# Kernel tuning notes

Measured on AMD Instinct MI355X. Metric: run time of the kernel, lower is better.

The kernel has to match this reference:

```python
import jax, jax.numpy as jnp
import numpy as np

N_QUBITS = 8
N_LAYERS = 3
N_FEATURES = 16
BATCH = 65536
DIM = 2 ** N_QUBITS  # 256 amplitudes
EPS = 1e-5  # torch BatchNorm1d default eps

# Precompute CNOT permutations (wire 0 = most significant bit, PennyLane order)
_idx = np.arange(DIM)
CNOT_PERMS = []
for _i in range(N_QUBITS):
    for _j in range(_i + 1, N_QUBITS):
        _c = (_idx >> (N_QUBITS - 1 - _i)) & 1
        CNOT_PERMS.append(np.where(_c == 1, _idx ^ (1 << (N_QUBITS - 1 - _j)), _idx))
# PauliZ sign table: (DIM, N_QUBITS), +1 for bit 0, -1 for bit 1
Z_SIGNS = np.stack([1.0 - 2.0 * ((_idx >> (N_QUBITS - 1 - i)) & 1) for i in range(N_QUBITS)], axis=1).astype(np.float32)


def _ry(theta):
    t = jnp.asarray(theta)
    c = jnp.cos(t / 2).astype(jnp.complex64)
    s = jnp.sin(t / 2).astype(jnp.complex64)
    return jnp.stack([jnp.stack([c, -s], -1), jnp.stack([s, c], -1)], -2)


def _rx(theta):
    t = jnp.asarray(theta)
    c = jnp.cos(t / 2).astype(jnp.complex64)
    s = (-1j) * jnp.sin(t / 2).astype(jnp.complex64)
    return jnp.stack([jnp.stack([c, s], -1), jnp.stack([s, c], -1)], -2)


def _rz(theta):
    e = jnp.exp(-0.5j * jnp.asarray(theta, jnp.complex64))
    z = jnp.zeros_like(e)
    return jnp.stack([jnp.stack([e, z], -1), jnp.stack([z, jnp.conj(e)], -1)], -2)


def _apply_1q(state, U, w):
    # state: (B, DIM); U: (2,2) shared or (B,2,2) per-sample; wire w
    B = state.shape[0]
    left, right = 2 ** w, 2 ** (N_QUBITS - 1 - w)
    s = state.reshape(B, left, 2, right)
    if U.ndim == 2:
        out = jnp.einsum('st,bpsq->bptq', U, s)
    else:
        out = jnp.einsum('bst,bpsq->bptq', U, s)
    return out.reshape(B, DIM)


def _quantum(angles, qw):
    # Batched state-vector simulation of the PennyLane circuit.
    # angles: (B, N_QUBITS) float32 encoding angles; qw: (N_LAYERS, N_QUBITS, 3)
    B = angles.shape[0]
    state = jnp.zeros((B, DIM), jnp.complex64).at[:, 0].set(1.0 + 0.0j)
    for i in range(N_QUBITS):  # RY(inputs[i]) encoding, per-sample angles
        state = _apply_1q(state, _ry(angles[:, i]), i)
    for l in range(N_LAYERS):
        for i in range(N_QUBITS):
            state = _apply_1q(state, _rx(qw[l, i, 0]), i)
            state = _apply_1q(state, _ry(qw[l, i, 1]), i)
            state = _apply_1q(state, _rz(qw[l, i, 2]), i)
        for perm in CNOT_PERMS:  # all-pairs CNOT(i, j), i < j
            state = state[:, perm]
    probs = state.real ** 2 + state.imag ** 2  # (B, DIM)
    return probs @ jnp.asarray(Z_SIGNS)  # (B, N_QUBITS) <Z_i> expectations


def _bn(h, g, b, m, v):
    # BatchNorm1d in inference mode (running stats)
    return (h - m) * jax.lax.rsqrt(v + EPS) * g + b


def _forward(x, W1, b1, g1, bt1, m1, v1, W2, b2, g2, bt2, m2, v2, W3, b3, q_weights, W4, b4, g4, bt4, m4, v4, W5, b5, W6, b6):
    h = jax.nn.relu(_bn(x @ W1.T + b1, g1, bt1, m1, v1))
    h = jax.nn.relu(_bn(h @ W2.T + b2, g2, bt2, m2, v2))
    pre = jnp.tanh(h @ W3.T + b3)  # (B, N_QUBITS)
    # Original detaches before the quantum circuit -> no grad through it
    q_out = _quantum(jax.lax.stop_gradient(pre), jax.lax.stop_gradient(q_weights))
    h = jax.nn.relu(_bn(q_out @ W4.T + b4, g4, bt4, m4, v4))
    h = jax.nn.relu(h @ W5.T + b5)
    return h @ W6.T + b6  # (B, 1)


def setup_inputs() -> dict:
    key = jax.random.key(0)
    ks = jax.random.split(key, 8)

    def lin(k, o, i):
        return (jax.random.normal(k, (o, i), jnp.float32) / np.sqrt(i)).astype(jnp.float32)

    return {
        'x': jax.random.normal(ks[0], (BATCH, N_FEATURES), jnp.float32),
        'W1': lin(ks[1], 128, N_FEATURES), 'b1': jnp.zeros((128,), jnp.float32),
        'g1': jnp.ones((128,), jnp.float32), 'bt1': jnp.zeros((128,), jnp.float32),
        'm1': jnp.zeros((128,), jnp.float32), 'v1': jnp.ones((128,), jnp.float32),
        'W2': lin(ks[2], 64, 128), 'b2': jnp.zeros((64,), jnp.float32),
        'g2': jnp.ones((64,), jnp.float32), 'bt2': jnp.zeros((64,), jnp.float32),
        'm2': jnp.zeros((64,), jnp.float32), 'v2': jnp.ones((64,), jnp.float32),
        'W3': lin(ks[3], N_QUBITS, 64), 'b3': jnp.zeros((N_QUBITS,), jnp.float32),
        'q_weights': jax.random.normal(ks[4], (N_LAYERS, N_QUBITS, 3), jnp.float32) * 0.1,
        'W4': lin(ks[5], 32, N_QUBITS), 'b4': jnp.zeros((32,), jnp.float32),
        'g4': jnp.ones((32,), jnp.float32), 'bt4': jnp.zeros((32,), jnp.float32),
        'm4': jnp.zeros((32,), jnp.float32), 'v4': jnp.ones((32,), jnp.float32),
        'W5': lin(ks[6], 16, 32), 'b5': jnp.zeros((16,), jnp.float32),
        'W6': lin(ks[7], 1, 16), 'b6': jnp.zeros((1,), jnp.float32),
    }


def reference(x, W1, b1, g1, bt1, m1, v1, W2, b2, g2, bt2, m2, v2, W3, b3, q_weights, W4, b4, g4, bt4, m4, v4, W5, b5, W6, b6):
    return _forward(x, W1, b1, g1, bt1, m1, v1, W2, b2, g2, bt2, m2, v2, W3, b3, q_weights, W4, b4, g4, bt4, m4, v4, W5, b5, W6, b6)
```

## Files before the change

kernel.cpp:

```cpp
#include <hip/hip_runtime.h>

__device__ __forceinline__ float2 cmul(float2 a, float2 b){
    return make_float2(a.x*b.x - a.y*b.y, a.x*b.y + a.y*b.x);
}
__device__ __forceinline__ float2 cadd(float2 a, float2 b){
    return make_float2(a.x + b.x, a.y + b.y);
}
__device__ __forceinline__ unsigned short f2h(float f){
    _Float16 h = (_Float16)f;
    return __builtin_bit_cast(unsigned short, h);
}

typedef _Float16 f16x8 __attribute__((ext_vector_type(8)));
typedef float    f32x4 __attribute__((ext_vector_type(4)));

__device__ __forceinline__ void split8(const float* p, f16x8& ah, f16x8& al){
    const f32x4* q = (const f32x4*)p;
    f32x4 v0 = q[0], v1 = q[1];
    float av[8] = {v0[0],v0[1],v0[2],v0[3],v1[0],v1[1],v1[2],v1[3]};
    #pragma unroll
    for (int j=0;j<8;++j){
        _Float16 h = (_Float16)av[j];
        ah[j] = h;
        al[j] = (_Float16)(av[j] - (float)h);
    }
}

__device__ __forceinline__ void build_gates(const float* qw, int l, int c, float2 (*G)[2][2]){
    if (c < 8){
        int i = c;
        float t0 = 0.5f*qw[l*24 + i*3 + 0];
        float t1 = 0.5f*qw[l*24 + i*3 + 1];
        float t2 = 0.5f*qw[l*24 + i*3 + 2];
        float c1,s1,c2,s2,c3,s3;
        sincosf(t0,&s1,&c1); sincosf(t1,&s2,&c2); sincosf(t2,&s3,&c3);
        float2 RX[2][2] = {{{c1,0.f},{0.f,-s1}},{{0.f,-s1},{c1,0.f}}};
        float2 RY[2][2] = {{{c2,0.f},{s2,0.f}},{{-s2,0.f},{c2,0.f}}};
        float2 M[2][2];
        #pragma unroll
        for (int r=0;r<2;++r)
            #pragma unroll
            for (int cc=0;cc<2;++cc)
                M[r][cc] = cadd(cmul(RY[r][0],RX[0][cc]), cmul(RY[r][1],RX[1][cc]));
        float2 e  = {c3,-s3};
        float2 ec = {c3, s3};
        G[i][0][0]=cmul(e, M[0][0]); G[i][0][1]=cmul(e, M[0][1]);
        G[i][1][0]=cmul(ec,M[1][0]); G[i][1][1]=cmul(ec,M[1][1]);
    }
}
__device__ __forceinline__ int cnot_perm(int k){
    int r = k;
    for (int i=6;i>=0;--i)
        for (int j=7;j>i;--j)
            if ((r >> (7-i)) & 1) r ^= 1 << (7-j);
    return r;
}

__global__ void k_build_prep(const float* __restrict__ qw, float2* __restrict__ U,
                       const float* __restrict__ W1, const float* __restrict__ b1,
                       const float* __restrict__ g1, const float* __restrict__ bt1,
                       const float* __restrict__ m1, const float* __restrict__ v1,
                       const float* __restrict__ W2, const float* __restrict__ b2,
                       const float* __restrict__ g2, const float* __restrict__ bt2,
                       const float* __restrict__ m2, const float* __restrict__ v2,
                       const float* __restrict__ W3,
                       unsigned short* __restrict__ H1w, float* __restrict__ c1,
                       unsigned short* __restrict__ H2w, float* __restrict__ c2,
                       unsigned short* __restrict__ H3w){
    if (blockIdx.y == 2){
        if (blockIdx.x >= 8) return;
        int tid = blockIdx.x*256 + threadIdx.x;
        const int stride = 8*256;
        for (int i=tid; i<4096; i+=stride){ int n=i>>5, k=i&31;
            float s=g1[n]*rsqrtf(v1[n]+1e-5f);
            H1w[i] = f2h(k<16 ? W1[n*16+k]*s : 0.f); }
        for (int i=tid; i<128;  i+=stride){ float s=g1[i]*rsqrtf(v1[i]+1e-5f); c1[i]=(b1[i]-m1[i])*s+bt1[i]; }
        for (int i=tid; i<8192; i+=stride){ int n=i>>7;
            float s=g2[n]*rsqrtf(v2[n]+1e-5f);
            H2w[i] = f2h(W2[i]*s); }
        for (int i=tid; i<64;   i+=stride){ float s=g2[i]*rsqrtf(v2[i]+1e-5f); c2[i]=(b2[i]-m2[i])*s+bt2[i]; }
        for (int i=tid; i<1024; i+=stride){ int n=i>>6, k=i&63;
            H3w[i] = f2h(n<8 ? W3[n*64+k] : 0.f); }
        return;
    }
    __shared__ float2 G[8][2][2];
    int l = blockIdx.y, k = blockIdx.x, c = threadIdx.x;
    build_gates(qw, l, c, G);
    __syncthreads();
    int r = cnot_perm(k);
    float2 p = {1.f, 0.f};
    #pragma unroll
    for (int i=0;i<8;++i)
        p = cmul(p, G[i][(r>>(7-i))&1][(c>>(7-i))&1]);
    U[l*65536 + k*256 + c] = p;
}

__global__ __launch_bounds__(256) void k_rowmm(const float* __restrict__ qw,
                                              const float2* __restrict__ U,
                                              unsigned short* __restrict__ WqS){
    __shared__ float2 G[8][2][2];
    __shared__ float2 vs[256];
    __shared__ float2 ws[256];
    int r = blockIdx.x, c = threadIdx.x;
    build_gates(qw, 2, c, G);
    __syncthreads();
    int pr = cnot_perm(r);
    float2 p = {1.f, 0.f};
    #pragma unroll
    for (int i=0;i<8;++i)
        p = cmul(p, G[i][(pr>>(7-i))&1][(c>>(7-i))&1]);
    vs[c] = p;
    __syncthreads();
    float2 acc = {0.f,0.f};
    #pragma unroll 8
    for (int m=0;m<256;++m)
        acc = cadd(acc, cmul(vs[m], U[65536 + m*256 + c]));
    ws[c] = acc;
    __syncthreads();
    float2 z = {0.f,0.f};
    #pragma unroll 8
    for (int m=0;m<256;++m)
        z = cadd(z, cmul(ws[m], U[m*256 + c]));
    int T = r >> 4, l15 = r & 15;
    int ks = c >> 5, lq = (c >> 3) & 3, j = c & 7;
    int lane = lq*16 + l15;
    WqS[((T     *8 + ks)*64 + lane)*8 + j] = f2h(z.x);
    WqS[(((T+16)*8 + ks)*64 + lane)*8 + j] = f2h(z.y);
}

__global__ __launch_bounds__(256,2) void k_front(
    const float* __restrict__ x,
    const unsigned short* __restrict__ H1w, const float* __restrict__ c1,
    const unsigned short* __restrict__ H2w, const float* __restrict__ c2,
    const unsigned short* __restrict__ H3w, const float* __restrict__ b3,
    float* __restrict__ pre)
{
    __shared__ __align__(16) char smem[60416];
    float* XS = (float*)smem;
    float* H1 = (float*)(smem + 9216);
    float* H2 = (float*)(smem + 43008);

    int tid = threadIdx.x;
    int row0 = blockIdx.x*64;
    {
        int r = tid >> 2, q = tid & 3;
        const float4* xp = (const float4*)(x + (row0 + r)*16 + q*4);
        float4 v = xp[0];
        *(float4*)(XS + r*36 + q*4) = v;
        *(float4*)(XS + r*36 + 16 + q*4) = make_float4(0.f,0.f,0.f,0.f);
    }
    __syncthreads();

    int wave = tid>>6, lane = tid&63, l15 = lane&15, lq = lane>>4;
    const f32x4 zz = {0.f,0.f,0.f,0.f};

    f32x4 acc1[4][2];
    #pragma unroll
    for (int mt=0;mt<4;++mt){ acc1[mt][0]=zz; acc1[mt][1]=zz; }
    #pragma unroll
    for (int mt=0; mt<4; ++mt){
        f16x8 ah, al;
        split8(XS + (mt*16+l15)*36 + lq*8, ah, al);
        #pragma unroll
        for (int t=0;t<2;++t){
            int nt = wave + t*4;
            f16x8 b = *(const f16x8*)(H1w + (nt*16+l15)*32 + lq*8);
            acc1[mt][t] = __builtin_amdgcn_mfma_f32_16x16x32_f16(ah, b, acc1[mt][t], 0,0,0);
            acc1[mt][t] = __builtin_amdgcn_mfma_f32_16x16x32_f16(al, b, acc1[mt][t], 0,0,0);
        }
    }
    #pragma unroll
    for (int t=0;t<2;++t){
        int n = (wave + t*4)*16 + l15;
        float bias = c1[n];
        #pragma unroll
        for (int mt=0; mt<4; ++mt)
            #pragma unroll
            for (int reg=0; reg<4; ++reg){
                int rowl = mt*16 + lq*4 + reg;
                H1[rowl*132 + n] = fmaxf(acc1[mt][t][reg] + bias, 0.f);
            }
    }
    __syncthreads();

    f32x4 acc2[4];
    #pragma unroll
    for (int mt=0;mt<4;++mt) acc2[mt]=zz;
    #pragma unroll
    for (int ks=0; ks<4; ++ks){
        f16x8 b = *(const f16x8*)(H2w + (wave*16+l15)*128 + ks*32 + lq*8);
        #pragma unroll
        for (int mt=0; mt<4; ++mt){
            f16x8 ah, al;
            split8(H1 + (mt*16+l15)*132 + ks*32 + lq*8, ah, al);
            acc2[mt] = __builtin_amdgcn_mfma_f32_16x16x32_f16(ah, b, acc2[mt], 0,0,0);
            acc2[mt] = __builtin_amdgcn_mfma_f32_16x16x32_f16(al, b, acc2[mt], 0,0,0);
        }
    }
    {
        int n = wave*16 + l15;
        float bias = c2[n];
        #pragma unroll
        for (int mt=0; mt<4; ++mt)
            #pragma unroll
            for (int reg=0; reg<4; ++reg){
                int rowl = mt*16 + lq*4 + reg;
                H2[rowl*68 + n] = fmaxf(acc2[mt][reg] + bias, 0.f);
            }
    }
    __syncthreads();

    f32x4 acc3 = zz;
    #pragma unroll
    for (int ks=0; ks<2; ++ks){
        f16x8 b = *(const f16x8*)(H3w + l15*64 + ks*32 + lq*8);
        f16x8 ah, al;
        split8(H2 + (wave*16+l15)*68 + ks*32 + lq*8, ah, al);
        acc3 = __builtin_amdgcn_mfma_f32_16x16x32_f16(ah, b, acc3, 0,0,0);
        acc3 = __builtin_amdgcn_mfma_f32_16x16x32_f16(al, b, acc3, 0,0,0);
    }
    if (l15 < 8){
        float bias = b3[l15];
        #pragma unroll
        for (int reg=0; reg<4; ++reg){
            int rowl = wave*16 + lq*4 + reg;
            pre[(row0+rowl)*8 + l15] = tanhf(acc3[reg] + bias);
        }
    }
}

#define A_STRIDE 264
#define P_STRIDE 268
__global__ __launch_bounds__(256,2) void k_main(
    const float* __restrict__ pre, const unsigned short* __restrict__ WqS,
    const float* __restrict__ W4, const float* __restrict__ b4, const float* __restrict__ g4,
    const float* __restrict__ bt4, const float* __restrict__ m4, const float* __restrict__ v4,
    const float* __restrict__ W5, const float* __restrict__ b5,
    const float* __restrict__ W6, const float* __restrict__ b6,
    float* __restrict__ out)
{
    __shared__ __align__(16) char smem[34304 + 4096 + 2048];
    unsigned short* As = (unsigned short*)smem;
    float* probs = (float*)smem;
    float* qacc  = (float*)(smem + 34304);
    float* qout  = (float*)(smem + 34304 + 4096);

    int tid = threadIdx.x;
    {
        int row = tid & 63, q = tid >> 6;
        int grow = blockIdx.x*64 + row;
        const float4* p4 = (const float4*)(pre + grow*8);
        float4 pa = p4[0], pb = p4[1];
        float th[8] = {pa.x,pa.y,pa.z,pa.w,pb.x,pb.y,pb.z,pb.w};
        float cs[8], sn[8];
        #pragma unroll
        for (int i=0;i<8;++i){ __sincosf(0.5f*th[i], &sn[i], &cs[i]); sn[i] = -sn[i]; }
        float F = (q&2 ? sn[0] : cs[0]) * (q&1 ? sn[1] : cs[1]);
        float Pm[8], Pl[8];
        #pragma unroll
        for (int a2=0;a2<8;++a2){
            Pm[a2] = (a2&4?sn[2]:cs[2]) * (a2&2?sn[3]:cs[3]) * (a2&1?sn[4]:cs[4]);
            Pl[a2] = (a2&4?sn[5]:cs[5]) * (a2&2?sn[6]:cs[6]) * (a2&1?sn[7]:cs[7]);
        }
        unsigned short* arow = As + row*A_STRIDE + q*64;
        #pragma unroll
        for (int mh=0;mh<8;++mh){
            float fm = F * Pm[mh];
            uint4 w;
            w.x = (unsigned)f2h(fm*Pl[0]) | ((unsigned)f2h(fm*Pl[1])<<16);
            w.y = (unsigned)f2h(fm*Pl[2]) | ((unsigned)f2h(fm*Pl[3])<<16);
            w.z = (unsigned)f2h(fm*Pl[4]) | ((unsigned)f2h(fm*Pl[5])<<16);
            w.w = (unsigned)f2h(fm*Pl[6]) | ((unsigned)f2h(fm*Pl[7])<<16);
            *reinterpret_cast<uint4*>(arow + mh*8) = w;
        }
    }
    __syncthreads();

    int wave = tid >> 6, lane = tid & 63;
    int l15 = lane & 15, lq = lane >> 4;

    const f16x8* Bp[8];
    #pragma unroll
    for (int t=0;t<8;++t){
        int T = ((t>>2)<<4) + wave*4 + (t&3);
        Bp[t] = reinterpret_cast<const f16x8*>(WqS + T*4096) + lane;
    }
    const f16x8* Ap[4];
    #pragma unroll
    for (int mt=0;mt<4;++mt)
        Ap[mt] = reinterpret_cast<const f16x8*>(As + (mt*16 + l15)*A_STRIDE + lq*8);

    f32x4 acc[4][8];
    const f32x4 zz = {0.f,0.f,0.f,0.f};
    #pragma unroll
    for (int mt=0;mt<4;++mt)
        #pragma unroll
        for (int t=0;t<8;++t) acc[mt][t] = zz;

    f16x8 bfr[2][8];
    #pragma unroll
    for (int t=0;t<8;++t) bfr[0][t] = Bp[t][0];

    #pragma unroll
    for (int ks=0;ks<8;++ks){
        int cur = ks & 1;
        if (ks < 7){
            #pragma unroll
            for (int t=0;t<8;++t) bfr[cur^1][t] = Bp[t][(ks+1)*64];
        }
        f16x8 afr[4];
        #pragma unroll
        for (int mt=0;mt<4;++mt) afr[mt] = Ap[mt][ks*4];
        #pragma unroll
        for (int mt=0;mt<4;++mt)
            #pragma unroll
            for (int t=0;t<8;++t)
                acc[mt][t] = __builtin_amdgcn_mfma_f32_16x16x32_f16(afr[mt], bfr[cur][t], acc[mt][t], 0, 0, 0);
    }
    __syncthreads();

    #pragma unroll
    for (int h=0; h<2; ++h){
        #pragma unroll
        for (int mtl=0; mtl<2; ++mtl){
            int mt = h*2 + mtl;
            #pragma unroll
            for (int t=0;t<4;++t){
                #pragma unroll
                for (int reg=0;reg<4;++reg){
                    float sr = acc[mt][t][reg];
                    float si = acc[mt][t+4][reg];
                    int prow = mtl*16 + lq*4 + reg;
                    int pcol = wave*64 + t*16 + l15;
                    probs[prow*P_STRIDE + pcol] = fmaf(sr,sr,si*si);
                }
            }
        }
        __syncthreads();
        if (tid < 128){
            int row = tid & 31, kg = tid >> 5;
            const float* pb = probs + row*P_STRIDE + kg*64;
            float S=0.f,q2=0.f,q3=0.f,q4=0.f,q5=0.f,q6=0.f,q7=0.f;
            #pragma unroll
            for (int j=0;j<64;++j){
                float p = pb[j];
                S  += p;
                q2 += (j&32)? -p : p;
                q3 += (j&16)? -p : p;
                q4 += (j&8) ? -p : p;
                q5 += (j&4) ? -p : p;
                q6 += (j&2) ? -p : p;
                q7 += (j&1) ? -p : p;
            }
            float* qa = qacc + tid*8;
            qa[0] = (kg&2)? -S : S;
            qa[1] = (kg&1)? -S : S;
            qa[2]=q2; qa[3]=q3; qa[4]=q4; qa[5]=q5; qa[6]=q6; qa[7]=q7;
        }
        __syncthreads();
        {
            int r = tid >> 3, i = tid & 7;
            float v = qacc[r*8+i] + qacc[(32+r)*8+i] + qacc[(64+r)*8+i] + qacc[(96+r)*8+i];
            qout[(h*32 + r)*8 + i] = v;
        }
    }
    __syncthreads();

    if (tid < 64){
        int r = tid;
        float qv[8];
        #pragma unroll
        for (int i=0;i<8;++i) qv[i] = qout[r*8+i];
        float h4[32];
        #pragma unroll
        for (int j=0;j<32;++j){
            float a = b4[j];
            #pragma unroll
            for (int i=0;i<8;++i) a = fmaf(qv[i], W4[j*8+i], a);
            float sc = g4[j]*rsqrtf(v4[j]+1e-5f);
            a = fmaf(a - m4[j], sc, bt4[j]);
            h4[j] = fmaxf(a, 0.f);
        }
        float h5[16];
        #pragma unroll
        for (int j=0;j<16;++j){
            float a = b5[j];
            #pragma unroll
            for (int k=0;k<32;++k) a = fmaf(h4[k], W5[j*32+k], a);
            h5[j] = fmaxf(a, 0.f);
        }
        float o = b6[0];
        #pragma unroll
        for (int k=0;k<16;++k) o = fmaf(h5[k], W6[k], o);
        out[blockIdx.x*64 + r] = o;
    }
}

extern "C" void kernel_launch(void* const* d_in, const int* in_sizes, int n_in,
                              void* d_out, int out_size, void* d_ws, size_t ws_size,
                              hipStream_t stream) {
    (void)in_sizes; (void)n_in; (void)out_size; (void)ws_size;
    const float* x   = (const float*)d_in[0];
    const float* W1  = (const float*)d_in[1];
    const float* b1  = (const float*)d_in[2];
    const float* g1  = (const float*)d_in[3];
    const float* bt1 = (const float*)d_in[4];
    const float* m1  = (const float*)d_in[5];
    const float* v1  = (const float*)d_in[6];
    const float* W2  = (const float*)d_in[7];
    const float* b2  = (const float*)d_in[8];
    const float* g2  = (const float*)d_in[9];
    const float* bt2 = (const float*)d_in[10];
    const float* m2  = (const float*)d_in[11];
    const float* v2  = (const float*)d_in[12];
    const float* W3  = (const float*)d_in[13];
    const float* b3  = (const float*)d_in[14];
    const float* qw  = (const float*)d_in[15];
    const float* W4  = (const float*)d_in[16];
    const float* b4  = (const float*)d_in[17];
    const float* g4  = (const float*)d_in[18];
    const float* bt4 = (const float*)d_in[19];
    const float* m4  = (const float*)d_in[20];
    const float* v4  = (const float*)d_in[21];
    const float* W5  = (const float*)d_in[22];
    const float* b5  = (const float*)d_in[23];
    const float* W6  = (const float*)d_in[24];
    const float* b6  = (const float*)d_in[25];

    char* ws = (char*)d_ws;
    float2* U   = (float2*)ws;
    unsigned short* WqS = (unsigned short*)(U + 2*65536);
    float* pre  = (float*)(WqS + 512*256);
    unsigned short* H1w = (unsigned short*)(pre + 65536*8);
    unsigned short* H2w = H1w + 4096;
    unsigned short* H3w = H2w + 8192;
    float* c1 = (float*)(H3w + 1024);
    float* c2 = c1 + 128;

    k_build_prep<<<dim3(256,3), 256, 0, stream>>>(qw, U,
                                  W1,b1,g1,bt1,m1,v1, W2,b2,g2,bt2,m2,v2, W3,
                                  H1w,c1,H2w,c2,H3w);
    k_rowmm<<<256, 256, 0, stream>>>(qw, U, WqS);
    k_front<<<1024, 256, 0, stream>>>(x, H1w,c1, H2w,c2, H3w,b3, pre);
    k_main<<<1024, 256, 0, stream>>>(pre, WqS, W4,b4,g4,bt4,m4,v4, W5,b5,W6,b6,
                                     (float*)d_out);
}
```

Before: 183.3 us.

## Fuse front MLP and quantum main kernels into one kernel

Merges k_front and k_main into a single kernel that keeps the tanh encoding angles in shared memory, so the intermediate pre buffer no longer makes a round trip through global memory and one launch is dropped. Shared memory is aliased across stages, which needs extra barriers. The PauliZ reduction now uses all 256 threads over 32-column chunks with vector stores and an 8-way sum. The risks are higher LDS use (about 62KB per block), which may limit occupancy, and a longer kernel with more register pressure.

```diff
diff --git a/kernel.cpp b/kernel.cpp
--- a/kernel.cpp
+++ b/kernel.cpp
@@ -128,20 +128,35 @@
     WqS[(((T+16)*8 + ks)*64 + lane)*8 + j] = f2h(z.y);
 }
 
-__global__ __launch_bounds__(256,2) void k_front(
+#define A_STRIDE 264
+#define P_STRIDE 269
+__global__ __launch_bounds__(256,2) void k_fused(
     const float* __restrict__ x,
     const unsigned short* __restrict__ H1w, const float* __restrict__ c1,
     const unsigned short* __restrict__ H2w, const float* __restrict__ c2,
     const unsigned short* __restrict__ H3w, const float* __restrict__ b3,
-    float* __restrict__ pre)
+    const unsigned short* __restrict__ WqS,
+    const float* __restrict__ W4, const float* __restrict__ b4, const float* __restrict__ g4,
+    const float* __restrict__ bt4, const float* __restrict__ m4, const float* __restrict__ v4,
+    const float* __restrict__ W5, const float* __restrict__ b5,
+    const float* __restrict__ W6, const float* __restrict__ b6,
+    float* __restrict__ out)
 {
-    __shared__ __align__(16) char smem[60416];
-    float* XS = (float*)smem;
-    float* H1 = (float*)(smem + 9216);
-    float* H2 = (float*)(smem + 43008);
+    __shared__ __align__(16) char smem[62464];
+    float* XS   = (float*)smem;
+    float* H1   = (float*)(smem + 9216);
+    float* H2   = (float*)(smem + 43008);
+    float* preL = (float*)(smem + 60416);
+    unsigned short* As = (unsigned short*)smem;
+    float* probs = (float*)smem;
+    float* qacc  = (float*)(smem + 34432);
+    float* qout  = (float*)(smem + 42624);
 
     int tid = threadIdx.x;
     int row0 = blockIdx.x*64;
+    int wave = tid>>6, lane = tid&63, l15 = lane&15, lq = lane>>4;
+    const f32x4 zz = {0.f,0.f,0.f,0.f};
+
     {
         int r = tid >> 2, q = tid & 3;
         const float4* xp = (const float4*)(x + (row0 + r)*16 + q*4);
@@ -151,53 +166,53 @@
     }
     __syncthreads();
 
-    int wave = tid>>6, lane = tid&63, l15 = lane&15, lq = lane>>4;
-    const f32x4 zz = {0.f,0.f,0.f,0.f};
-
-    f32x4 acc1[4][2];
-    #pragma unroll
-    for (int mt=0;mt<4;++mt){ acc1[mt][0]=zz; acc1[mt][1]=zz; }
-    #pragma unroll
-    for (int mt=0; mt<4; ++mt){
-        f16x8 ah, al;
-        split8(XS + (mt*16+l15)*36 + lq*8, ah, al);
-        #pragma unroll
-        for (int t=0;t<2;++t){
-            int nt = wave + t*4;
-            f16x8 b = *(const f16x8*)(H1w + (nt*16+l15)*32 + lq*8);
-            acc1[mt][t] = __builtin_amdgcn_mfma_f32_16x16x32_f16(ah, b, acc1[mt][t], 0,0,0);
-            acc1[mt][t] = __builtin_amdgcn_mfma_f32_16x16x32_f16(al, b, acc1[mt][t], 0,0,0);
-        }
-    }
-    #pragma unroll
-    for (int t=0;t<2;++t){
-        int n = (wave + t*4)*16 + l15;
-        float bias = c1[n];
-        #pragma unroll
-        for (int mt=0; mt<4; ++mt)
-            #pragma unroll
-            for (int reg=0; reg<4; ++reg){
-                int rowl = mt*16 + lq*4 + reg;
-                H1[rowl*132 + n] = fmaxf(acc1[mt][t][reg] + bias, 0.f);
-            }
-    }
-    __syncthreads();
-
-    f32x4 acc2[4];
-    #pragma unroll
-    for (int mt=0;mt<4;++mt) acc2[mt]=zz;
-    #pragma unroll
-    for (int ks=0; ks<4; ++ks){
-        f16x8 b = *(const f16x8*)(H2w + (wave*16+l15)*128 + ks*32 + lq*8);
+    {
+        f32x4 acc1[4][2];
+        #pragma unroll
+        for (int mt=0;mt<4;++mt){ acc1[mt][0]=zz; acc1[mt][1]=zz; }
         #pragma unroll
         for (int mt=0; mt<4; ++mt){
             f16x8 ah, al;
-            split8(H1 + (mt*16+l15)*132 + ks*32 + lq*8, ah, al);
-            acc2[mt] = __builtin_amdgcn_mfma_f32_16x16x32_f16(ah, b, acc2[mt], 0,0,0);
-            acc2[mt] = __builtin_amdgcn_mfma_f32_16x16x32_f16(al, b, acc2[mt], 0,0,0);
-        }
-    }
+            split8(XS + (mt*16+l15)*36 + lq*8, ah, al);
+            #pragma unroll
+            for (int t=0;t<2;++t){
+                int nt = wave + t*4;
+                f16x8 b = *(const f16x8*)(H1w + (nt*16+l15)*32 + lq*8);
+                acc1[mt][t] = __builtin_amdgcn_mfma_f32_16x16x32_f16(ah, b, acc1[mt][t], 0,0,0);
+                acc1[mt][t] = __builtin_amdgcn_mfma_f32_16x16x32_f16(al, b, acc1[mt][t], 0,0,0);
+            }
+        }
+        __syncthreads();
+        #pragma unroll
+        for (int t=0;t<2;++t){
+            int n = (wave + t*4)*16 + l15;
+            float bias = c1[n];
+            #pragma unroll
+            for (int mt=0; mt<4; ++mt)
+                #pragma unroll
+                for (int reg=0; reg<4; ++reg){
+                    int rowl = mt*16 + lq*4 + reg;
+                    H1[rowl*132 + n] = fmaxf(acc1[mt][t][reg] + bias, 0.f);
+                }
+        }
+    }
+    __syncthreads();
+
     {
+        f32x4 acc2[4];
+        #pragma unroll
+        for (int mt=0;mt<4;++mt) acc2[mt]=zz;
+        #pragma unroll
+        for (int ks=0; ks<4; ++ks){
+            f16x8 b = *(const f16x8*)(H2w + (wave*16+l15)*128 + ks*32 + lq*8);
+            #pragma unroll
+            for (int mt=0; mt<4; ++mt){
+                f16x8 ah, al;
+                split8(H1 + (mt*16+l15)*132 + ks*32 + lq*8, ah, al);
+                acc2[mt] = __builtin_amdgcn_mfma_f32_16x16x32_f16(ah, b, acc2[mt], 0,0,0);
+                acc2[mt] = __builtin_amdgcn_mfma_f32_16x16x32_f16(al, b, acc2[mt], 0,0,0);
+            }
+        }
         int n = wave*16 + l15;
         float bias = c2[n];
         #pragma unroll
@@ -210,46 +225,30 @@
     }
     __syncthreads();
 
-    f32x4 acc3 = zz;
-    #pragma unroll
-    for (int ks=0; ks<2; ++ks){
-        f16x8 b = *(const f16x8*)(H3w + l15*64 + ks*32 + lq*8);
-        f16x8 ah, al;
-        split8(H2 + (wave*16+l15)*68 + ks*32 + lq*8, ah, al);
-        acc3 = __builtin_amdgcn_mfma_f32_16x16x32_f16(ah, b, acc3, 0,0,0);
-        acc3 = __builtin_amdgcn_mfma_f32_16x16x32_f16(al, b, acc3, 0,0,0);
-    }
-    if (l15 < 8){
-        float bias = b3[l15];
-        #pragma unroll
-        for (int reg=0; reg<4; ++reg){
-            int rowl = wave*16 + lq*4 + reg;
-            pre[(row0+rowl)*8 + l15] = tanhf(acc3[reg] + bias);
-        }
-    }
-}
-
-#define A_STRIDE 264
-#define P_STRIDE 268
-__global__ __launch_bounds__(256,2) void k_main(
-    const float* __restrict__ pre, const unsigned short* __restrict__ WqS,
-    const float* __restrict__ W4, const float* __restrict__ b4, const float* __restrict__ g4,
-    const float* __restrict__ bt4, const float* __restrict__ m4, const float* __restrict__ v4,
-    const float* __restrict__ W5, const float* __restrict__ b5,
-    const float* __restrict__ W6, const float* __restrict__ b6,
-    float* __restrict__ out)
-{
-    __shared__ __align__(16) char smem[34304 + 4096 + 2048];
-    unsigned short* As = (unsigned short*)smem;
-    float* probs = (float*)smem;
-    float* qacc  = (float*)(smem + 34304);
-    float* qout  = (float*)(smem + 34304 + 4096);
-
-    int tid = threadIdx.x;
+    {
+        f32x4 acc3 = zz;
+        #pragma unroll
+        for (int ks=0; ks<2; ++ks){
+            f16x8 b = *(const f16x8*)(H3w + l15*64 + ks*32 + lq*8);
+            f16x8 ah, al;
+            split8(H2 + (wave*16+l15)*68 + ks*32 + lq*8, ah, al);
+            acc3 = __builtin_amdgcn_mfma_f32_16x16x32_f16(ah, b, acc3, 0,0,0);
+            acc3 = __builtin_amdgcn_mfma_f32_16x16x32_f16(al, b, acc3, 0,0,0);
+        }
+        if (l15 < 8){
+            float bias = b3[l15];
+            #pragma unroll
+            for (int reg=0; reg<4; ++reg){
+                int rowl = wave*16 + lq*4 + reg;
+                preL[rowl*8 + l15] = tanhf(acc3[reg] + bias);
+            }
+        }
+    }
+    __syncthreads();
+
     {
         int row = tid & 63, q = tid >> 6;
-        int grow = blockIdx.x*64 + row;
-        const float4* p4 = (const float4*)(pre + grow*8);
+        const float4* p4 = (const float4*)(preL + row*8);
         float4 pa = p4[0], pb = p4[1];
         float th[8] = {pa.x,pa.y,pa.z,pa.w,pb.x,pb.y,pb.z,pb.w};
         float cs[8], sn[8];
@@ -262,6 +261,7 @@
             Pm[a2] = (a2&4?sn[2]:cs[2]) * (a2&2?sn[3]:cs[3]) * (a2&1?sn[4]:cs[4]);
             Pl[a2] = (a2&4?sn[5]:cs[5]) * (a2&2?sn[6]:cs[6]) * (a2&1?sn[7]:cs[7]);
         }
+        __syncthreads();
         unsigned short* arow = As + row*A_STRIDE + q*64;
         #pragma unroll
         for (int mh=0;mh<8;++mh){
@@ -276,9 +276,6 @@
     }
     __syncthreads();
 
-    int wave = tid >> 6, lane = tid & 63;
-    int l15 = lane & 15, lq = lane >> 4;
-
     const f16x8* Bp[8];
     #pragma unroll
     for (int t=0;t<8;++t){
@@ -291,7 +288,6 @@
         Ap[mt] = reinterpret_cast<const f16x8*>(As + (mt*16 + l15)*A_STRIDE + lq*8);
 
     f32x4 acc[4][8];
-    const f32x4 zz = {0.f,0.f,0.f,0.f};
     #pragma unroll
     for (int mt=0;mt<4;++mt)
         #pragma unroll
@@ -337,30 +333,35 @@
             }
         }
         __syncthreads();
-        if (tid < 128){
-            int row = tid & 31, kg = tid >> 5;
-            const float* pb = probs + row*P_STRIDE + kg*64;
-            float S=0.f,q2=0.f,q3=0.f,q4=0.f,q5=0.f,q6=0.f,q7=0.f;
-            #pragma unroll
-            for (int j=0;j<64;++j){
+        {
+            int row = tid & 31, q = tid >> 5;
+            const float* pb = probs + row*P_STRIDE + q*32;
+            float S=0.f,z3=0.f,z4=0.f,z5=0.f,z6=0.f,z7=0.f;
+            #pragma unroll
+            for (int j=0;j<32;++j){
                 float p = pb[j];
                 S  += p;
-                q2 += (j&32)? -p : p;
-                q3 += (j&16)? -p : p;
-                q4 += (j&8) ? -p : p;
-                q5 += (j&4) ? -p : p;
-                q6 += (j&2) ? -p : p;
-                q7 += (j&1) ? -p : p;
-            }
-            float* qa = qacc + tid*8;
-            qa[0] = (kg&2)? -S : S;
-            qa[1] = (kg&1)? -S : S;
-            qa[2]=q2; qa[3]=q3; qa[4]=q4; qa[5]=q5; qa[6]=q6; qa[7]=q7;
+                z3 += (j&16)? -p : p;
+                z4 += (j&8) ? -p : p;
+                z5 += (j&4) ? -p : p;
+                z6 += (j&2) ? -p : p;
+                z7 += (j&1) ? -p : p;
+            }
+            float* qa = qacc + (q*32 + row)*8;
+            f32x4 w0 = { (q&4)? -S : S,
+                         (q&2)? -S : S,
+                         (q&1)? -S : S,
+                         z3 };
+            f32x4 w1 = { z4, z5, z6, z7 };
+            *(f32x4*)qa = w0;
+            *(f32x4*)(qa+4) = w1;
         }
         __syncthreads();
         {
             int r = tid >> 3, i = tid & 7;
-            float v = qacc[r*8+i] + qacc[(32+r)*8+i] + qacc[(64+r)*8+i] + qacc[(96+r)*8+i];
+            float v = 0.f;
+            #pragma unroll
+            for (int g=0; g<8; ++g) v += qacc[(g*32 + r)*8 + i];
             qout[(h*32 + r)*8 + i] = v;
         }
     }
@@ -430,8 +431,7 @@
     char* ws = (char*)d_ws;
     float2* U   = (float2*)ws;
     unsigned short* WqS = (unsigned short*)(U + 2*65536);
-    float* pre  = (float*)(WqS + 512*256);
-    unsigned short* H1w = (unsigned short*)(pre + 65536*8);
+    unsigned short* H1w = WqS + 512*256;
     unsigned short* H2w = H1w + 4096;
     unsigned short* H3w = H2w + 8192;
     float* c1 = (float*)(H3w + 1024);
@@ -441,7 +441,7 @@
                                   W1,b1,g1,bt1,m1,v1, W2,b2,g2,bt2,m2,v2, W3,
                                   H1w,c1,H2w,c2,H3w);
     k_rowmm<<<256, 256, 0, stream>>>(qw, U, WqS);
-    k_front<<<1024, 256, 0, stream>>>(x, H1w,c1, H2w,c2, H3w,b3, pre);
-    k_main<<<1024, 256, 0, stream>>>(pre, WqS, W4,b4,g4,bt4,m4,v4, W5,b5,W6,b6,
-                                     (float*)d_out);
-}
+    k_fused<<<1024, 256, 0, stream>>>(x, H1w,c1, H2w,c2, H3w,b3, WqS,
+                                      W4,b4,g4,bt4,m4,v4, W5,b5,W6,b6,
+                                      (float*)d_out);
+}
```

After: 184.6 us. No clear change (+0.7%).
